# Kernel optimization log

Hardware: AMD Instinct MI355X
Metric: run time of the kernel (lower is better)

Reference implementation:

```python
import jax, jax.numpy as jnp
import numpy as np

N = 1_000_000  # nodes
K = 32         # kNN neighbors
NU = 3


def setup_inputs() -> dict:
    key = jax.random.key(0)
    k1, k2, k3 = jax.random.split(key, 3)
    indices = jax.random.randint(k1, (N, K), 0, N, dtype=jnp.int32)
    distances = jax.random.uniform(k2, (N, K), dtype=jnp.float32)
    x = jax.random.normal(k3, (N,), dtype=jnp.float32)
    eps = jnp.float32(0.1)   # eps_ parameter
    k = jnp.float32(1.0)     # k_ parameter
    return {"x": x, "indices": indices, "distances": distances,
            "eps": eps, "k": k, "nu": NU}


def _build_laplacian(indices, distances, eps, k, nu):
    # Gaussian kernel weights over kNN edges
    w = jnp.exp(-distances / eps)                      # [N,K]
    D = w.sum(axis=1)                                  # [N]
    w = w / D[:, None] / D[indices]                    # bi-stochastic-ish normalization
    w = -w / w.sum(axis=1, keepdims=True)              # row-normalized, negated
    n = indices.shape[0]
    vals = jnp.concatenate([jnp.ones((n, 1), w.dtype), w], axis=1) * (4.0 / eps)
    vals = vals.at[:, 0].add(2.0 * nu / (k ** 2) + 10.0)   # [N,K+1]
    idx = jnp.concatenate(
        [jnp.arange(n, dtype=indices.dtype)[:, None], indices], axis=1)  # [N,K+1]
    return vals, idx


def reference(x, indices, distances, eps, k, nu):
    vals, idx = _build_laplacian(indices, distances, eps, k, nu)
    y = x
    for _ in range(nu):  # nu is a small static int (Matern order)
        # gather-weighted-sum over self + K neighbors per node
        y = jnp.sum(vals * y[idx], axis=1)  # [N]
    return jnp.dot(x, y)  # scalar quadratic form x^T L^nu x
```

## Files before the change

kernel.cpp:

```cpp
#include <hip/hip_runtime.h>
#include <hip/hip_fp16.h>


typedef float __attribute__((ext_vector_type(4))) floatx4;
typedef unsigned int uint32;

static constexpr int BLOCK = 256;

__global__ __launch_bounds__(256) void dinv_kernel(
    const float* __restrict__ dist, const float* __restrict__ x,
    const float* __restrict__ eps_p,
    __half2* __restrict__ z4, int n_edges) {
  int t = blockIdx.x * BLOCK + threadIdx.x;
  int e4 = t << 2;
  if (e4 >= n_edges) return;
  float inv_eps = 1.0f / eps_p[0];
  floatx4 d = __builtin_nontemporal_load((const floatx4*)(dist + e4));
  float s = __expf(-d.x * inv_eps) + __expf(-d.y * inv_eps) +
            __expf(-d.z * inv_eps) + __expf(-d.w * inv_eps);
  #pragma unroll
  for (int off = 4; off > 0; off >>= 1) s += __shfl_down(s, off, 8);
  if ((t & 7) == 0) {
    int node = t >> 3;
    z4[node] = __halves2half2(__float2half(1.0f / s), __float2half(x[node]));
  }
}

__global__ __launch_bounds__(256) void fsweep_kernel(
    const float* __restrict__ dist, const int* __restrict__ nbr,
    const __half2* __restrict__ z4,
    const float* __restrict__ x, const float* __restrict__ eps_p,
    const float* __restrict__ k_p, const int* __restrict__ nu_p,
    uint32* __restrict__ pk, float* __restrict__ yout, int n_edges) {
  int e = blockIdx.x * BLOCK + threadIdx.x;
  if (e >= n_edges) return;
  float inv_eps = 1.0f / eps_p[0];
  int j = __builtin_nontemporal_load(nbr + e);
  float d = __builtin_nontemporal_load(dist + e);
  __half2 z = z4[j];
  float t = __expf(-d * inv_eps) * __low2float(z);
  float g = t * __high2float(z);
  float s = t;
  #pragma unroll
  for (int off = 1; off < 32; off <<= 1) s += __shfl_xor(s, off, 32);
  uint32 mq = (uint32)__float2uint_rn(t * (4096.0f / s));
  if (mq > 4095u) mq = 4095u;
  __builtin_nontemporal_store(((uint32)j << 12) | mq, pk + e);
  #pragma unroll
  for (int off = 16; off > 0; off >>= 1) g += __shfl_down(g, off, 32);
  if ((threadIdx.x & 31) == 0) {
    int node = e >> 5;
    float kk = k_p[0];
    float a = 4.0f * inv_eps + 2.0f * (float)nu_p[0] / (kk * kk) + 10.0f;
    float b = -4.0f * inv_eps;
    yout[node] = a * x[node] + b * g / s;
  }
}

template <bool LAST>
__global__ __launch_bounds__(256) void sweep_kernel(
    const uint32* __restrict__ pk,
    const float* __restrict__ yin, float* __restrict__ yout,
    const float* __restrict__ x,
    const float* __restrict__ eps_p, const float* __restrict__ k_p,
    const int* __restrict__ nu_p,
    float* __restrict__ out, int n_edges) {
  __shared__ float bsum;
  if (LAST) { if (threadIdx.x == 0) bsum = 0.0f; __syncthreads(); }
  float inv_eps = 1.0f / eps_p[0];
  float kk = k_p[0];
  float a  = 4.0f * inv_eps + 2.0f * (float)nu_p[0] / (kk * kk) + 10.0f;
  float bq = -4.0f * inv_eps * (1.0f / 4096.0f);
  int stride = gridDim.x * BLOCK;
  for (int e = blockIdx.x * BLOCK + threadIdx.x; e < n_edges; e += stride) {
    uint32 p = __builtin_nontemporal_load(pk + e);
    float g = (float)(p & 0xFFFu) * yin[p >> 12];
    #pragma unroll
    for (int off = 16; off > 0; off >>= 1) g += __shfl_down(g, off, 32);
    if ((threadIdx.x & 31) == 0) {
      int node = e >> 5;
      float ynew = a * yin[node] + bq * g;
      if (LAST) atomicAdd(&bsum, x[node] * ynew);
      else yout[node] = ynew;
    }
  }
  if (LAST) { __syncthreads(); if (threadIdx.x == 0) atomicAdd(out, bsum); }
}

extern "C" void kernel_launch(void* const* d_in, const int* in_sizes, int n_in,
                              void* d_out, int out_size, void* d_ws, size_t ws_size,
                              hipStream_t stream) {
  const float* x     = (const float*)d_in[0];
  const int*   nbr   = (const int*)d_in[1];
  const float* dist  = (const float*)d_in[2];
  const float* eps_p = (const float*)d_in[3];
  const float* k_p   = (const float*)d_in[4];
  const int*   nu_p  = (const int*)d_in[5];
  float* out = (float*)d_out;

  int n  = in_sizes[0];
  int ne = in_sizes[1];

  uint32* pk   = (uint32*)d_ws;
  __half2* z4  = (__half2*)(pk + ne);
  float* y1    = (float*)(z4 + n);
  float* y2    = y1 + n;

  (void)hipMemsetAsync(d_out, 0, sizeof(float), stream);

  int gridE = (ne + BLOCK - 1) / BLOCK;
  int grid4 = (ne + BLOCK * 4 - 1) / (BLOCK * 4);
  dinv_kernel<<<grid4, BLOCK, 0, stream>>>(dist, x, eps_p, z4, ne);
  fsweep_kernel<<<gridE, BLOCK, 0, stream>>>(dist, nbr, z4, x, eps_p, k_p, nu_p, pk, y1, ne);
  sweep_kernel<false><<<gridE, BLOCK, 0, stream>>>(pk, y1, y2, x, eps_p, k_p, nu_p, out, ne);
  sweep_kernel<true ><<<gridE / 8, BLOCK, 0, stream>>>(pk, y2, nullptr, x, eps_p, k_p, nu_p, out, ne);
}
```

Before: 891.6 us.

## Fuse all stages into one cooperative persistent kernel with grid syncs

Replaces the four separate launches (degree pass, first sweep, two packed sweeps) with a single cooperative kernel that runs all stages in grid-stride loops and separates them with grid.sync(). The grid size comes from an occupancy query times 256 CUs, with the old multi-kernel path kept as a fallback if the cooperative launch fails. The aim is to remove inter-kernel launch gaps and tail effects, at the cost of grid-wide barriers and fewer resident threads to hide gather latency. The final reduction now accumulates per lane before the shared atomic, and the division by s becomes a reciprocal multiply.

```diff
diff --git a/kernel.cpp b/kernel.cpp
--- a/kernel.cpp
+++ b/kernel.cpp
@@ -1,11 +1,100 @@
 #include <hip/hip_runtime.h>
 #include <hip/hip_fp16.h>
+#include <hip/hip_cooperative_groups.h>
+
+namespace cg = cooperative_groups;
 
 
 typedef float __attribute__((ext_vector_type(4))) floatx4;
 typedef unsigned int uint32;
 
 static constexpr int BLOCK = 256;
+
+__global__ __launch_bounds__(256, 8) void mega_kernel(
+    const float* __restrict__ x, const int* __restrict__ nbr,
+    const float* __restrict__ dist,
+    const float* __restrict__ eps_p, const float* __restrict__ k_p,
+    const int* __restrict__ nu_p,
+    uint32* __restrict__ pk, __half2* __restrict__ z4,
+    float* __restrict__ y1, float* __restrict__ y2,
+    float* __restrict__ out, int n_edges) {
+  cg::grid_group grid = cg::this_grid();
+  __shared__ float bsum;
+  const int tid = blockIdx.x * BLOCK + threadIdx.x;
+  const int nth = gridDim.x * BLOCK;
+  const float inv_eps = 1.0f / eps_p[0];
+  const float kk = k_p[0];
+  const float a = 4.0f * inv_eps + 2.0f * (float)nu_p[0] / (kk * kk) + 10.0f;
+  const float b = -4.0f * inv_eps;
+  const float bq = b * (1.0f / 4096.0f);
+
+  if (tid == 0) *out = 0.0f;
+
+  const int nq = n_edges >> 2;
+  for (int t = tid; t < nq; t += nth) {
+    floatx4 d = __builtin_nontemporal_load((const floatx4*)(dist + (t << 2)));
+    float s = __expf(-d.x * inv_eps) + __expf(-d.y * inv_eps) +
+              __expf(-d.z * inv_eps) + __expf(-d.w * inv_eps);
+    #pragma unroll
+    for (int off = 4; off > 0; off >>= 1) s += __shfl_down(s, off, 8);
+    if ((t & 7) == 0) {
+      int node = t >> 3;
+      z4[node] = __halves2half2(__float2half(1.0f / s), __float2half(x[node]));
+    }
+  }
+  grid.sync();
+
+  for (int e = tid; e < n_edges; e += nth) {
+    int j = __builtin_nontemporal_load(nbr + e);
+    float d = __builtin_nontemporal_load(dist + e);
+    __half2 z = z4[j];
+    float t = __expf(-d * inv_eps) * __low2float(z);
+    float g = t * __high2float(z);
+    float s = t;
+    #pragma unroll
+    for (int off = 1; off < 32; off <<= 1) s += __shfl_xor(s, off, 32);
+    float inv_s = 1.0f / s;
+    uint32 mq = (uint32)__float2uint_rn(t * 4096.0f * inv_s);
+    if (mq > 4095u) mq = 4095u;
+    __builtin_nontemporal_store(((uint32)j << 12) | mq, pk + e);
+    #pragma unroll
+    for (int off = 16; off > 0; off >>= 1) g += __shfl_down(g, off, 32);
+    if ((threadIdx.x & 31) == 0) {
+      int node = e >> 5;
+      y1[node] = a * x[node] + b * g * inv_s;
+    }
+  }
+  grid.sync();
+
+  for (int e = tid; e < n_edges; e += nth) {
+    uint32 p = __builtin_nontemporal_load(pk + e);
+    float g = (float)(p & 0xFFFu) * y1[p >> 12];
+    #pragma unroll
+    for (int off = 16; off > 0; off >>= 1) g += __shfl_down(g, off, 32);
+    if ((threadIdx.x & 31) == 0) {
+      int node = e >> 5;
+      y2[node] = a * y1[node] + bq * g;
+    }
+  }
+  grid.sync();
+
+  if (threadIdx.x == 0) bsum = 0.0f;
+  __syncthreads();
+  float acc = 0.0f;
+  for (int e = tid; e < n_edges; e += nth) {
+    uint32 p = __builtin_nontemporal_load(pk + e);
+    float g = (float)(p & 0xFFFu) * y2[p >> 12];
+    #pragma unroll
+    for (int off = 16; off > 0; off >>= 1) g += __shfl_down(g, off, 32);
+    if ((threadIdx.x & 31) == 0) {
+      int node = e >> 5;
+      acc += x[node] * (a * y2[node] + bq * g);
+    }
+  }
+  if ((threadIdx.x & 31) == 0) atomicAdd(&bsum, acc);
+  __syncthreads();
+  if (threadIdx.x == 0) atomicAdd(out, bsum);
+}
 
 __global__ __launch_bounds__(256) void dinv_kernel(
     const float* __restrict__ dist, const float* __restrict__ x,
@@ -43,7 +132,8 @@
   float s = t;
   #pragma unroll
   for (int off = 1; off < 32; off <<= 1) s += __shfl_xor(s, off, 32);
-  uint32 mq = (uint32)__float2uint_rn(t * (4096.0f / s));
+  float inv_s = 1.0f / s;
+  uint32 mq = (uint32)__float2uint_rn(t * 4096.0f * inv_s);
   if (mq > 4095u) mq = 4095u;
   __builtin_nontemporal_store(((uint32)j << 12) | mq, pk + e);
   #pragma unroll
@@ -53,7 +143,7 @@
     float kk = k_p[0];
     float a = 4.0f * inv_eps + 2.0f * (float)nu_p[0] / (kk * kk) + 10.0f;
     float b = -4.0f * inv_eps;
-    yout[node] = a * x[node] + b * g / s;
+    yout[node] = a * x[node] + b * g * inv_s;
   }
 }
 
@@ -108,10 +198,27 @@
 
   (void)hipMemsetAsync(d_out, 0, sizeof(float), stream);
 
-  int gridE = (ne + BLOCK - 1) / BLOCK;
-  int grid4 = (ne + BLOCK * 4 - 1) / (BLOCK * 4);
-  dinv_kernel<<<grid4, BLOCK, 0, stream>>>(dist, x, eps_p, z4, ne);
-  fsweep_kernel<<<gridE, BLOCK, 0, stream>>>(dist, nbr, z4, x, eps_p, k_p, nu_p, pk, y1, ne);
-  sweep_kernel<false><<<gridE, BLOCK, 0, stream>>>(pk, y1, y2, x, eps_p, k_p, nu_p, out, ne);
-  sweep_kernel<true ><<<gridE / 8, BLOCK, 0, stream>>>(pk, y2, nullptr, x, eps_p, k_p, nu_p, out, ne);
-}
+  static int grid_co = 0;
+  if (grid_co == 0) {
+    int nb = 0;
+    if (hipOccupancyMaxActiveBlocksPerMultiprocessor(&nb, mega_kernel, BLOCK, 0)
+            != hipSuccess || nb < 1)
+      nb = 4;
+    grid_co = nb * 256;
+  }
+
+  void* args[] = {(void*)&x, (void*)&nbr, (void*)&dist, (void*)&eps_p,
+                  (void*)&k_p, (void*)&nu_p, (void*)&pk, (void*)&z4,
+                  (void*)&y1, (void*)&y2, (void*)&out, (void*)&ne};
+  hipError_t cerr = hipLaunchCooperativeKernel(
+      mega_kernel, dim3(grid_co), dim3(BLOCK), args, 0, stream);
+
+  if (cerr != hipSuccess) {
+    int gridE = (ne + BLOCK - 1) / BLOCK;
+    int grid4 = (ne + BLOCK * 4 - 1) / (BLOCK * 4);
+    dinv_kernel<<<grid4, BLOCK, 0, stream>>>(dist, x, eps_p, z4, ne);
+    fsweep_kernel<<<gridE, BLOCK, 0, stream>>>(dist, nbr, z4, x, eps_p, k_p, nu_p, pk, y1, ne);
+    sweep_kernel<false><<<gridE, BLOCK, 0, stream>>>(pk, y1, y2, x, eps_p, k_p, nu_p, out, ne);
+    sweep_kernel<true ><<<gridE / 8, BLOCK, 0, stream>>>(pk, y2, nullptr, x, eps_p, k_p, nu_p, out, ne);
+  }
+}
```

Measured after the change: 1.569 ms. 76.0% more time.
